# Kernel optimization log

Hardware: AMD Instinct MI355X
Metric: run time of the kernel (lower is better)

The kernel has to match this reference:

```python
import jax, jax.numpy as jnp
import numpy as np

B, C, K, D_SUB = 32768, 32, 256, 16
D_IN, D_OUT = C * D_SUB, 512


def setup_inputs() -> dict:
    key = jax.random.key(0)
    k1, k2, k3 = jax.random.split(key, 3)
    inputs = jax.random.normal(k1, (B, C, D_SUB), dtype=jnp.float32)
    centroids = jax.random.normal(k2, (C, K, D_SUB), dtype=jnp.float32)
    W = jax.random.normal(k3, (D_IN, D_OUT), dtype=jnp.float32) * (1.0 / np.sqrt(D_IN))
    return {"inputs": inputs, "centroids": centroids, "W": W}


def reference(inputs, centroids, W):
    # dot-metric response: (B, C, K). Equivalent to
    # torch.matmul(inputs.transpose(0,1), centroids.transpose(1,2)).transpose(0,1)
    response = jnp.einsum('bcd,ckd->bck', inputs, centroids)
    neg_mse = jnp.max(response, axis=-1)            # (B, C)
    codes = jnp.argmax(response, axis=-1)           # (B, C) int
    # codebook gather: outputs[b,c] = centroids[c, codes[b,c]]
    outputs = centroids[jnp.arange(C), codes]       # (B, C, D_SUB)
    # tie_in_n_out straight-through: value equals `outputs` in forward
    product = outputs.reshape(-1, C * D_SUB) @ W    # (B, D_OUT); fc has no bias
    return product, -neg_mse, codes
```

## Files before the change

### kernel.cpp

```cpp
#include <hip/hip_runtime.h>


#define NB 32768
#define NC 32
#define NK 256
#define NDS 16
#define NDIN 512
#define NDOUT 512
#define CERT 0.004f

typedef __attribute__((ext_vector_type(8))) short s8v;
typedef __attribute__((ext_vector_type(4))) float f4v;
typedef __attribute__((ext_vector_type(4))) unsigned int u4v;

__device__ __forceinline__ unsigned short f2bf(float f) {
  unsigned int u = __float_as_uint(f);
  u += 0x7fffu + ((u >> 16) & 1u);
  return (unsigned short)(u >> 16);
}
__device__ __forceinline__ float bf2f(unsigned short h) {
  return __uint_as_float(((unsigned int)h) << 16);
}

#define CVTPK(d, lo, hi) \
  asm("v_cvt_pk_bf16_f32 %0, %1, %2" : "=v"(d) : "v"(lo), "v"(hi))

__device__ __forceinline__ void gload16(const void* g, void* l) {
  __builtin_amdgcn_global_load_lds(
      (const __attribute__((address_space(1))) void*)g,
      (__attribute__((address_space(3))) void*)l, 16, 0, 0);
}

__device__ __forceinline__ float dot16(const float* x, const float* cj) {
  float4 a0 = *(const float4*)(x + 0),  a1 = *(const float4*)(x + 4);
  float4 a2 = *(const float4*)(x + 8),  a3 = *(const float4*)(x + 12);
  float4 c0 = *(const float4*)(cj + 0), c1 = *(const float4*)(cj + 4);
  float4 c2 = *(const float4*)(cj + 8), c3 = *(const float4*)(cj + 12);
  float s = a0.x * c0.x;
  s = fmaf(a0.y, c0.y, s); s = fmaf(a0.z, c0.z, s); s = fmaf(a0.w, c0.w, s);
  s = fmaf(a1.x, c1.x, s); s = fmaf(a1.y, c1.y, s); s = fmaf(a1.z, c1.z, s); s = fmaf(a1.w, c1.w, s);
  s = fmaf(a2.x, c2.x, s); s = fmaf(a2.y, c2.y, s); s = fmaf(a2.z, c2.z, s); s = fmaf(a2.w, c2.w, s);
  s = fmaf(a3.x, c3.x, s); s = fmaf(a3.y, c3.y, s); s = fmaf(a3.z, c3.z, s); s = fmaf(a3.w, c3.w, s);
  return s;
}

__global__ __launch_bounds__(256) void k_prep(const float* __restrict__ W,
                                              const float* __restrict__ cents,
                                              unsigned short* __restrict__ Wt,
                                              unsigned short* __restrict__ centsH,
                                              unsigned short* __restrict__ centsP4) {
  const int t = threadIdx.x;
  const int bid = blockIdx.x;
  if (bid < 256) {
    __shared__ float tile[32][33];
    const int k0 = (bid >> 4) << 5;
    const int n0 = (bid & 15) << 5;
    const int tx = t & 31, ty = t >> 5;
#pragma unroll
    for (int i = 0; i < 4; ++i) {
      int r = ty + i * 8;
      tile[r][tx] = W[(size_t)(k0 + r) * NDOUT + n0 + tx];
    }
    __syncthreads();
#pragma unroll
    for (int i = 0; i < 4; ++i) {
      int r = ty + i * 8;
      Wt[(size_t)(n0 + r) * NDIN + k0 + tx] = f2bf(tile[tx][r]);
    }
  } else {
    const int c = bid - 256;
    const int k = t;
    const float* src = cents + ((size_t)c * NK + k) * NDS;
    unsigned short hi[16], lo[16];
#pragma unroll
    for (int j = 0; j < 4; ++j) {
      float4 v = *(const float4*)(src + j * 4);
      unsigned short h0 = f2bf(v.x), h1 = f2bf(v.y), h2 = f2bf(v.z), h3 = f2bf(v.w);
      hi[j * 4 + 0] = h0; hi[j * 4 + 1] = h1; hi[j * 4 + 2] = h2; hi[j * 4 + 3] = h3;
      lo[j * 4 + 0] = f2bf(v.x - bf2f(h0));
      lo[j * 4 + 1] = f2bf(v.y - bf2f(h1));
      lo[j * 4 + 2] = f2bf(v.z - bf2f(h2));
      lo[j * 4 + 3] = f2bf(v.w - bf2f(h3));
    }
    unsigned short* hf = centsH + ((size_t)c * NK + k) * NDS;
#pragma unroll
    for (int j = 0; j < 4; ++j)
      *(ushort4*)(hf + j * 4) = make_ushort4(hi[j * 4], hi[j * 4 + 1], hi[j * 4 + 2], hi[j * 4 + 3]);
    unsigned short* pb = centsP4 + (size_t)c * 8192 + k * 8;
    *(ushort4*)(pb + 0 * 2048 + 0) = make_ushort4(hi[0], hi[1], hi[2], hi[3]);
    *(ushort4*)(pb + 0 * 2048 + 4) = make_ushort4(hi[4], hi[5], hi[6], hi[7]);
    *(ushort4*)(pb + 1 * 2048 + 0) = make_ushort4(hi[8], hi[9], hi[10], hi[11]);
    *(ushort4*)(pb + 1 * 2048 + 4) = make_ushort4(hi[12], hi[13], hi[14], hi[15]);
    *(ushort4*)(pb + 2 * 2048 + 0) = make_ushort4(lo[0], lo[1], lo[2], lo[3]);
    *(ushort4*)(pb + 2 * 2048 + 4) = make_ushort4(lo[4], lo[5], lo[6], lo[7]);
    *(ushort4*)(pb + 3 * 2048 + 0) = make_ushort4(lo[8], lo[9], lo[10], lo[11]);
    *(ushort4*)(pb + 3 * 2048 + 4) = make_ushort4(lo[12], lo[13], lo[14], lo[15]);
  }
}

__device__ __forceinline__ void split8(float4 u0, float4 u1, s8v& bh, s8v& bl) {
  unsigned int ph0, ph1, ph2, ph3;
  CVTPK(ph0, u0.x, u0.y); CVTPK(ph1, u0.z, u0.w);
  CVTPK(ph2, u1.x, u1.y); CVTPK(ph3, u1.z, u1.w);
  bh = __builtin_bit_cast(s8v, (u4v){ph0, ph1, ph2, ph3});
  float ra = u0.x - __uint_as_float(ph0 << 16);
  float rb = u0.y - __uint_as_float(ph0 & 0xFFFF0000u);
  float rc = u0.z - __uint_as_float(ph1 << 16);
  float rd = u0.w - __uint_as_float(ph1 & 0xFFFF0000u);
  float re = u1.x - __uint_as_float(ph2 << 16);
  float rf = u1.y - __uint_as_float(ph2 & 0xFFFF0000u);
  float rg = u1.z - __uint_as_float(ph3 << 16);
  float rh = u1.w - __uint_as_float(ph3 & 0xFFFF0000u);
  unsigned int pl0, pl1, pl2, pl3;
  CVTPK(pl0, ra, rb); CVTPK(pl1, rc, rd);
  CVTPK(pl2, re, rf); CVTPK(pl3, rg, rh);
  bl = __builtin_bit_cast(s8v, (u4v){pl0, pl1, pl2, pl3});
}

#define TRACK2(v0, v1, kc0, best, sec, bk)                     \
  {                                                            \
    float vm_ = fmaxf(v0, v1);                                 \
    float md_ = __builtin_amdgcn_fmed3f(best, v0, v1);         \
    sec = fmaxf(sec, md_);                                     \
    int km_ = (v1 > v0) ? (kc0 + 1) : (kc0);                   \
    bool gt_ = vm_ > best;                                     \
    bk = gt_ ? km_ : bk;                                       \
    best = fmaxf(best, vm_);                                   \
  }

__global__ __launch_bounds__(256, 4) void k_score(const float* __restrict__ inputs,
                                                  const unsigned short* __restrict__ centsP4,
                                                  const float* __restrict__ cents,
                                                  float* __restrict__ T_neg,
                                                  int* __restrict__ T_code) {
  const int t = threadIdx.x;
  const int l = t & 63;
  const int w = t >> 6;
  const int c = blockIdx.y;
  const int b0 = blockIdx.x * 128 + w * 32;
  const int g = l >> 4;
  const int col = l & 15;
  const int dh = (g & 1) * 8;
  const int g4 = g * 4;

  const unsigned short* abase = centsP4 + (size_t)c * 8192 + g * 2048 + col * 8;
  s8v areg[16];
#pragma unroll
  for (int kt = 0; kt < 16; ++kt)
    areg[kt] = *(const s8v*)(abase + kt * 128);

  s8v p1f0, p2f0, p1f1, p2f1;
  {
    const float* r0 = inputs + ((size_t)(b0 + col) * NC + c) * NDS + dh;
    const float* r1 = inputs + ((size_t)(b0 + 16 + col) * NC + c) * NDS + dh;
    float4 u0 = *(const float4*)(r0), u1 = *(const float4*)(r0 + 4);
    float4 v0 = *(const float4*)(r1), v1 = *(const float4*)(r1 + 4);
    s8v bh0, bl0, bh1, bl1;
    split8(u0, u1, bh0, bl0);
    split8(v0, v1, bh1, bl1);
    const bool hiLane = (l < 32);
    p1f0 = hiLane ? bh0 : bl0;
    p2f0 = hiLane ? bl0 : bh0;
    p1f1 = hiLane ? bh1 : bl1;
    p2f1 = hiLane ? bl1 : bh1;
  }

  float best0 = -3.0e38f, sec0 = -3.0e38f;
  float best1 = -3.0e38f, sec1 = -3.0e38f;
  int bk0 = 0, bk1 = 0;
  const f4v zz = {0.0f, 0.0f, 0.0f, 0.0f};

#pragma unroll
  for (int kt = 0; kt < 16; ++kt) {
    s8v a = areg[kt];
    f4v acc0 = __builtin_amdgcn_mfma_f32_16x16x32_bf16(a, p1f0, zz, 0, 0, 0);
    acc0 = __builtin_amdgcn_mfma_f32_16x16x32_bf16(a, p2f0, acc0, 0, 0, 0);
    f4v acc1 = __builtin_amdgcn_mfma_f32_16x16x32_bf16(a, p1f1, zz, 0, 0, 0);
    acc1 = __builtin_amdgcn_mfma_f32_16x16x32_bf16(a, p2f1, acc1, 0, 0, 0);
    const int kc = kt * 16;
    TRACK2(acc0[0], acc0[1], kc + 0, best0, sec0, bk0)
    TRACK2(acc0[2], acc0[3], kc + 2, best0, sec0, bk0)
    TRACK2(acc1[0], acc1[1], kc + 0, best1, sec1, bk1)
    TRACK2(acc1[2], acc1[3], kc + 2, best1, sec1, bk1)
  }

  bk0 += g4;
  bk1 += g4;

#pragma unroll
  for (int off = 16; off <= 32; off <<= 1) {
    float vb = __shfl_xor(best0, off);
    float sb = __shfl_xor(sec0, off);
    int kb = __shfl_xor(bk0, off);
    float mn = fminf(best0, vb);
    sec0 = fmaxf(fmaxf(sec0, sb), mn);
    bool take = (vb > best0) || (vb == best0 && kb < bk0);
    bk0 = take ? kb : bk0;
    best0 = fmaxf(best0, vb);

    vb = __shfl_xor(best1, off);
    sb = __shfl_xor(sec1, off);
    kb = __shfl_xor(bk1, off);
    mn = fminf(best1, vb);
    sec1 = fmaxf(fmaxf(sec1, sb), mn);
    take = (vb > best1) || (vb == best1 && kb < bk1);
    bk1 = take ? kb : bk1;
    best1 = fmaxf(best1, vb);
  }

  const int sub = (l >> 4) & 1;
  float best = sub ? best1 : best0;
  float sec = sub ? sec1 : sec0;
  int bk = sub ? bk1 : bk0;
  const bool owner = (l < 32);
  const bool flagged = owner && (best - sec <= CERT);

  if (owner && !flagged) {
    const int b = b0 + l;
    const float* xr = inputs + ((size_t)b * NC + c) * NDS;
    const float* cr = cents + ((size_t)c * NK + bk) * NDS;
    size_t o = (size_t)c * NB + b;
    T_neg[o] = dot16(xr, cr);
    T_code[o] = bk;
  }

  unsigned long long mask = __ballot(flagged);
  while (mask) {
    const int p = __builtin_ctzll(mask);
    mask &= mask - 1;
    const int b = b0 + p;
    const float* xr = inputs + ((size_t)b * NC + c) * NDS;
    const float* cr = cents + ((size_t)c * NK + l * 4) * NDS;
    float rb = -3.0e38f;
    int rk = 0;
#pragma unroll
    for (int q = 0; q < 4; ++q) {
      float d = dot16(xr, cr + q * NDS);
      if (d > rb) { rb = d; rk = l * 4 + q; }
    }
#pragma unroll
    for (int off = 1; off <= 32; off <<= 1) {
      float vb = __shfl_xor(rb, off);
      int kb = __shfl_xor(rk, off);
      bool take = (vb > rb) || (vb == rb && kb < rk);
      rb = take ? vb : rb;
      rk = take ? kb : rk;
    }
    if (l == 0) {
      size_t o = (size_t)c * NB + b;
      T_neg[o] = rb;
      T_code[o] = rk;
    }
  }
}

__global__ __launch_bounds__(256) void k_finish(const float* __restrict__ T_neg,
                                                const int* __restrict__ T_code,
                                                float* __restrict__ negout,
                                                float* __restrict__ codefout) {
  __shared__ float sneg[64][33];
  __shared__ int scode[64][33];
  const int t = threadIdx.x;
  const int b0 = blockIdx.x * 64;

#pragma unroll
  for (int it = 0; it < 8; ++it) {
    int lin = it * 256 + t;
    int c = lin >> 6, bi = lin & 63;
    sneg[bi][c] = T_neg[(size_t)c * NB + b0 + bi];
    scode[bi][c] = T_code[(size_t)c * NB + b0 + bi];
  }
  __syncthreads();

#pragma unroll
  for (int it = 0; it < 8; ++it) {
    int lin = it * 256 + t;
    int bi = lin >> 5, c = lin & 31;
    size_t o = (size_t)(b0 + bi) * NC + c;
    negout[o] = -sneg[bi][c];
    codefout[o] = (float)scode[bi][c];
  }
}

__global__ __launch_bounds__(256) void k_gemm(const unsigned short* __restrict__ centsB,
                                              const int* __restrict__ T_code,
                                              const unsigned short* __restrict__ Wt,
                                              float* __restrict__ out) {
  __shared__ __align__(16) unsigned short As[128 * 64];
  __shared__ __align__(16) unsigned short Bs[128 * 64];
  __shared__ int lcode[128 * 33];

  const int t = threadIdx.x;
  const int l = t & 63;
  const int w = t >> 6;
  const int wm = w >> 1, wn = w & 1;
  const int m0 = blockIdx.x * 128;
  const int n0 = blockIdx.y * 128;

  {
    const int cc = t >> 3;
    const int ch = t & 7;
#pragma unroll
    for (int i = 0; i < 4; ++i) {
      int row0 = ch * 16 + i * 4;
      int4 v = *(const int4*)(T_code + (size_t)cc * NB + m0 + row0);
      lcode[(row0 + 0) * 33 + cc] = v.x;
      lcode[(row0 + 1) * 33 + cc] = v.y;
      lcode[(row0 + 2) * 33 + cc] = v.z;
      lcode[(row0 + 3) * 33 + cc] = v.w;
    }
  }

  f4v acc[4][4] = {};
  const int s = t & 7;
  const int rq = t >> 3;

  for (int kt = 0; kt < 8; ++kt) {
    __syncthreads();
    const int c0 = kt * 4;
#pragma unroll
    for (int i = 0; i < 4; ++i) {
      int lr = i * 32 + rq;
      int srcslot = s ^ (lr & 7);
      int cl = srcslot >> 1, half = srcslot & 1;
      int code = lcode[lr * 33 + c0 + cl];
      const unsigned short* gsrc =
          centsB + ((size_t)((c0 + cl) * NK + code) * NDS + half * 8);
      gload16(gsrc, (char*)As + i * 4096 + (w << 10));
    }
#pragma unroll
    for (int i = 0; i < 4; ++i) {
      int lr = i * 32 + rq;
      int k16 = s ^ (lr & 7);
      const unsigned short* gsrc = Wt + (size_t)(n0 + lr) * NDIN + kt * 64 + k16 * 8;
      gload16(gsrc, (char*)Bs + i * 4096 + (w << 10));
    }
    __syncthreads();

    s8v af[4][2], bfr[4][2];
#pragma unroll
    for (int mf = 0; mf < 4; ++mf)
#pragma unroll
      for (int ks = 0; ks < 2; ++ks) {
        int row = wm * 64 + mf * 16 + (l & 15);
        int slot = ks * 4 + (l >> 4);
        af[mf][ks] = *(const s8v*)((const char*)As + row * 128 + ((slot ^ (row & 7)) << 4));
      }
#pragma unroll
    for (int nf = 0; nf < 4; ++nf)
#pragma unroll
      for (int ks = 0; ks < 2; ++ks) {
        int row = wn * 64 + nf * 16 + (l & 15);
        int slot = ks * 4 + (l >> 4);
        bfr[nf][ks] = *(const s8v*)((const char*)Bs + row * 128 + ((slot ^ (row & 7)) << 4));
      }
#pragma unroll
    for (int ks = 0; ks < 2; ++ks)
#pragma unroll
      for (int mf = 0; mf < 4; ++mf)
#pragma unroll
        for (int nf = 0; nf < 4; ++nf)
          acc[mf][nf] = __builtin_amdgcn_mfma_f32_16x16x32_bf16(
              af[mf][ks], bfr[nf][ks], acc[mf][nf], 0, 0, 0);
  }

#pragma unroll
  for (int mf = 0; mf < 4; ++mf)
#pragma unroll
    for (int nf = 0; nf < 4; ++nf)
#pragma unroll
      for (int r = 0; r < 4; ++r) {
        int row = m0 + wm * 64 + mf * 16 + (l >> 4) * 4 + r;
        int col = n0 + wn * 64 + nf * 16 + (l & 15);
        out[(size_t)row * NDOUT + col] = acc[mf][nf][r];
      }
}

extern "C" void kernel_launch(void* const* d_in, const int* in_sizes, int n_in,
                              void* d_out, int out_size, void* d_ws, size_t ws_size,
                              hipStream_t stream) {
  const float* inputs = (const float*)d_in[0];
  const float* cents  = (const float*)d_in[1];
  const float* W      = (const float*)d_in[2];

  float* out = (float*)d_out;
  float* negout   = out + (size_t)NB * NDOUT;
  float* codefout = negout + (size_t)NB * NC;

  unsigned short* Wt      = (unsigned short*)d_ws;
  unsigned short* centsH  = (unsigned short*)((char*)d_ws + 512 * 1024);
  unsigned short* centsP4 = (unsigned short*)((char*)d_ws + (1 << 20));
  float* T_neg            = (float*)((char*)d_ws + 2 * (1 << 20));
  int* T_code             = (int*)((char*)d_ws + 6 * (1 << 20));

  k_prep<<<288, 256, 0, stream>>>(W, cents, Wt, centsH, centsP4);
  k_score<<<dim3(NB / 128, NC), 256, 0, stream>>>(inputs, centsP4, cents, T_neg, T_code);
  k_finish<<<NB / 64, 256, 0, stream>>>(T_neg, T_code, negout, codefout);
  k_gemm<<<dim3(NB / 128, NDOUT / 128), 256, 0, stream>>>(centsH, T_code, Wt, out);
}
```

Baseline: 104.8 us.

## Fuse finish transpose into GEMM and halve centroid register preload in scoring

```diff
diff --git a/kernel.cpp b/kernel.cpp
--- a/kernel.cpp
+++ b/kernel.cpp
@@ -128,7 +128,7 @@
     best = fmaxf(best, vm_);                                   \
   }
 
-__global__ __launch_bounds__(256, 4) void k_score(const float* __restrict__ inputs,
+__global__ __launch_bounds__(256, 5) void k_score(const float* __restrict__ inputs,
                                                   const unsigned short* __restrict__ centsP4,
                                                   const float* __restrict__ cents,
                                                   float* __restrict__ T_neg,
@@ -144,9 +144,9 @@
   const int g4 = g * 4;
 
   const unsigned short* abase = centsP4 + (size_t)c * 8192 + g * 2048 + col * 8;
-  s8v areg[16];
-#pragma unroll
-  for (int kt = 0; kt < 16; ++kt)
+  s8v areg[8];
+#pragma unroll
+  for (int kt = 0; kt < 8; ++kt)
     areg[kt] = *(const s8v*)(abase + kt * 128);
 
   s8v p1f0, p2f0, p1f1, p2f1;
@@ -171,8 +171,9 @@
   const f4v zz = {0.0f, 0.0f, 0.0f, 0.0f};
 
 #pragma unroll
-  for (int kt = 0; kt < 16; ++kt) {
+  for (int kt = 0; kt < 8; ++kt) {
     s8v a = areg[kt];
+    areg[kt] = *(const s8v*)(abase + (kt + 8) * 128);
     f4v acc0 = __builtin_amdgcn_mfma_f32_16x16x32_bf16(a, p1f0, zz, 0, 0, 0);
     acc0 = __builtin_amdgcn_mfma_f32_16x16x32_bf16(a, p2f0, acc0, 0, 0, 0);
     f4v acc1 = __builtin_amdgcn_mfma_f32_16x16x32_bf16(a, p1f1, zz, 0, 0, 0);
@@ -184,6 +185,20 @@
     TRACK2(acc1[2], acc1[3], kc + 2, best1, sec1, bk1)
   }
 
+#pragma unroll
+  for (int kt = 8; kt < 16; ++kt) {
+    s8v a = areg[kt - 8];
+    f4v acc0 = __builtin_amdgcn_mfma_f32_16x16x32_bf16(a, p1f0, zz, 0, 0, 0);
+    acc0 = __builtin_amdgcn_mfma_f32_16x16x32_bf16(a, p2f0, acc0, 0, 0, 0);
+    f4v acc1 = __builtin_amdgcn_mfma_f32_16x16x32_bf16(a, p1f1, zz, 0, 0, 0);
+    acc1 = __builtin_amdgcn_mfma_f32_16x16x32_bf16(a, p2f1, acc1, 0, 0, 0);
+    const int kc = kt * 16;
+    TRACK2(acc0[0], acc0[1], kc + 0, best0, sec0, bk0)
+    TRACK2(acc0[2], acc0[3], kc + 2, best0, sec0, bk0)
+    TRACK2(acc1[0], acc1[1], kc + 0, best1, sec1, bk1)
+    TRACK2(acc1[2], acc1[3], kc + 2, best1, sec1, bk1)
+  }
+
   bk0 += g4;
   bk1 += g4;
 
@@ -254,38 +269,13 @@
   }
 }
 
-__global__ __launch_bounds__(256) void k_finish(const float* __restrict__ T_neg,
-                                                const int* __restrict__ T_code,
-                                                float* __restrict__ negout,
-                                                float* __restrict__ codefout) {
-  __shared__ float sneg[64][33];
-  __shared__ int scode[64][33];
-  const int t = threadIdx.x;
-  const int b0 = blockIdx.x * 64;
-
-#pragma unroll
-  for (int it = 0; it < 8; ++it) {
-    int lin = it * 256 + t;
-    int c = lin >> 6, bi = lin & 63;
-    sneg[bi][c] = T_neg[(size_t)c * NB + b0 + bi];
-    scode[bi][c] = T_code[(size_t)c * NB + b0 + bi];
-  }
-  __syncthreads();
-
-#pragma unroll
-  for (int it = 0; it < 8; ++it) {
-    int lin = it * 256 + t;
-    int bi = lin >> 5, c = lin & 31;
-    size_t o = (size_t)(b0 + bi) * NC + c;
-    negout[o] = -sneg[bi][c];
-    codefout[o] = (float)scode[bi][c];
-  }
-}
-
 __global__ __launch_bounds__(256) void k_gemm(const unsigned short* __restrict__ centsB,
                                               const int* __restrict__ T_code,
+                                              const float* __restrict__ T_neg,
                                               const unsigned short* __restrict__ Wt,
-                                              float* __restrict__ out) {
+                                              float* __restrict__ out,
+                                              float* __restrict__ negout,
+                                              float* __restrict__ codefout) {
   __shared__ __align__(16) unsigned short As[128 * 64];
   __shared__ __align__(16) unsigned short Bs[128 * 64];
   __shared__ int lcode[128 * 33];
@@ -374,6 +364,33 @@
         int col = n0 + wn * 64 + nf * 16 + (l & 15);
         out[(size_t)row * NDOUT + col] = acc[mf][nf][r];
       }
+
+  if (blockIdx.y == 0) {
+    __syncthreads();
+    float* sf = (float*)As;
+    {
+      const int cc = t >> 3;
+      const int ch = t & 7;
+#pragma unroll
+      for (int i = 0; i < 4; ++i) {
+        int row0 = ch * 16 + i * 4;
+        float4 v = *(const float4*)(T_neg + (size_t)cc * NB + m0 + row0);
+        sf[(row0 + 0) * 32 + cc] = v.x;
+        sf[(row0 + 1) * 32 + cc] = v.y;
+        sf[(row0 + 2) * 32 + cc] = v.z;
+        sf[(row0 + 3) * 32 + cc] = v.w;
+      }
+    }
+    __syncthreads();
+#pragma unroll
+    for (int it = 0; it < 16; ++it) {
+      int lin = it * 256 + t;
+      int bi = lin >> 5, c2 = lin & 31;
+      size_t o = (size_t)(m0 + bi) * NC + c2;
+      negout[o] = -sf[bi * 32 + c2];
+      codefout[o] = (float)lcode[bi * 33 + c2];
+    }
+  }
 }
 
 extern "C" void kernel_launch(void* const* d_in, const int* in_sizes, int n_in,
@@ -395,6 +412,6 @@
 
   k_prep<<<288, 256, 0, stream>>>(W, cents, Wt, centsH, centsP4);
   k_score<<<dim3(NB / 128, NC), 256, 0, stream>>>(inputs, centsP4, cents, T_neg, T_code);
-  k_finish<<<NB / 64, 256, 0, stream>>>(T_neg, T_code, negout, codefout);
-  k_gemm<<<dim3(NB / 128, NDOUT / 128), 256, 0, stream>>>(centsH, T_code, Wt, out);
-}
+  k_gemm<<<dim3(NB / 128, NDOUT / 128), 256, 0, stream>>>(centsH, T_code, T_neg, Wt, out,
+                                                          negout, codefout);
+}
```

New measurement: 106.1 us. No clear change (+1.2%).
